# Optimization experiments

Hardware: AMD Instinct MI355X
Metric: run time of the kernel (lower is better)

Reference implementation:

```python
import jax, jax.numpy as jnp
import numpy as np

N_NODES = 50000
N_EDGES = 800000
IN_CH, HID, HEADS, OUT_CH = 16, 64, 4, 8
NEG_SLOPE = 0.2


def _add_self_loops(edge_index, num_nodes):
    loop = jnp.arange(num_nodes, dtype=edge_index.dtype)
    loops = jnp.stack([loop, loop])  # [2, N]
    return jnp.concatenate([edge_index, loops], axis=1)


def _gat_conv(x, src, dst, W, a_src, a_dst, bias, concat):
    """PyG-style GATConv: linear -> per-edge LeakyReLU attention -> segment
    softmax over incoming edges -> scatter-add aggregate."""
    N = x.shape[0]
    H, C = a_src.shape
    h = (x @ W).reshape(N, H, C)                      # [N,H,C]
    alpha_src = (h * a_src).sum(-1)                   # [N,H]
    alpha_dst = (h * a_dst).sum(-1)                   # [N,H]
    e = jax.nn.leaky_relu(alpha_src[src] + alpha_dst[dst], NEG_SLOPE)  # [E,H]
    # numerically stable segment softmax over edges grouped by dst
    e_max = jax.ops.segment_max(e, dst, num_segments=N)
    e_exp = jnp.exp(e - e_max[dst])
    denom = jax.ops.segment_sum(e_exp, dst, num_segments=N)
    alpha = e_exp / denom[dst]                        # [E,H]
    msg = h[src] * alpha[:, :, None]                  # [E,H,C]
    out = jax.ops.segment_sum(msg, dst, num_segments=N)  # [N,H,C]
    if concat:
        return out.reshape(N, H * C) + bias
    return out.mean(axis=1) + bias


def setup_inputs() -> dict:
    key = jax.random.key(0)
    ks = jax.random.split(key, 12)
    s = 0.1
    return {
        "x": jax.random.normal(ks[0], (N_NODES, IN_CH), jnp.float32),
        "edge_index": jax.random.randint(ks[1], (2, N_EDGES), 0, N_NODES, jnp.int64),
        "W1": jax.random.normal(ks[2], (IN_CH, HEADS * HID), jnp.float32) * s,
        "as1": jax.random.normal(ks[3], (HEADS, HID), jnp.float32) * s,
        "ad1": jax.random.normal(ks[4], (HEADS, HID), jnp.float32) * s,
        "b1": jnp.zeros((HEADS * HID,), jnp.float32),
        "W2": jax.random.normal(ks[5], (HEADS * HID, HEADS * HID), jnp.float32) * s,
        "as2": jax.random.normal(ks[6], (HEADS, HID), jnp.float32) * s,
        "ad2": jax.random.normal(ks[7], (HEADS, HID), jnp.float32) * s,
        "b2": jnp.zeros((HID,), jnp.float32),
        "Wc": jax.random.normal(ks[8], (HID, OUT_CH), jnp.float32) * s,
        "bc": jnp.zeros((OUT_CH,), jnp.float32),
    }


def reference(x, edge_index, W1, as1, ad1, b1, W2, as2, ad2, b2, Wc, bc):
    ei = _add_self_loops(edge_index, x.shape[0])
    src, dst = ei[0], ei[1]
    h = _gat_conv(x, src, dst, W1, as1, ad1, b1, concat=True)
    h = jax.nn.elu(h)
    h = _gat_conv(h, src, dst, W2, as2, ad2, b2, concat=False)
    h = jax.nn.elu(h)
    return h @ Wc + bc  # [N, OUT_CH]
```

## Files before the change

kernel.cpp:

```cpp
#include <hip/hip_runtime.h>
#include <math.h>

#define NODES   50000
#define HEADS   4
#define HID     64
#define FDIM    256
#define IN_CH   16
#define NEG_SLOPE 0.2f

typedef unsigned short ushort_t;
typedef unsigned int uint_t;
typedef __attribute__((ext_vector_type(8))) short bf16x8;
typedef __attribute__((ext_vector_type(4))) float f32x4;
typedef __attribute__((ext_vector_type(2))) float f32x2;

__device__ inline ushort_t f2bf(float f) {
    uint_t u = __float_as_uint(f);
    u += 0x7fffu + ((u >> 16) & 1u);
    return (ushort_t)(u >> 16);
}
__device__ inline void unpack2(uint_t u, float& a, float& b) {
    a = __uint_as_float(u << 16);
    b = __uint_as_float(u & 0xffff0000u);
}
__device__ inline uint_t f2h(float f) {
    _Float16 h = (_Float16)f;
    return (uint_t)*(ushort_t*)&h;
}
__device__ inline float h2f(uint_t u) {
    ushort_t us = (ushort_t)u;
    _Float16 h = *(_Float16*)&us;
    return (float)h;
}


__global__ __launch_bounds__(256) void k_prep(const float* __restrict__ x,
                                              const float* __restrict__ W1,
                                              const float* __restrict__ as1,
                                              const float* __restrict__ ad1,
                                              const float* __restrict__ W2,
                                              const int* __restrict__ ei, int E,
                                              ushort_t* __restrict__ h,
                                              float* __restrict__ asrc,
                                              float* __restrict__ adst,
                                              ushort_t* __restrict__ W2T,
                                              int* __restrict__ deg, int Nn) {
    int bid = blockIdx.x, t = threadIdx.x;
    if (bid >= Nn + 256) {
        int e = (bid - Nn - 256) * 256 + t;
        int Etot = E + Nn;
        if (e >= Etot) return;
        int d = (e < E) ? ei[E + e] : (e - E);
        if (d >= 0 && d < Nn) atomicAdd(&deg[d], 1);
        return;
    }
    if (bid >= Nn) {
        int idx = (bid - Nn) * 256 + t;
        int n = idx >> 8, k = idx & 255;
        W2T[idx] = f2bf(W2[k * FDIM + n]);
        return;
    }
    const float4* xp = (const float4*)(x + bid * IN_CH);
    float4 x0 = xp[0], x1 = xp[1], x2 = xp[2], x3 = xp[3];
    float s = x0.x * W1[t]            + x0.y * W1[FDIM + t]
            + x0.z * W1[2 * FDIM + t] + x0.w * W1[3 * FDIM + t]
            + x1.x * W1[4 * FDIM + t] + x1.y * W1[5 * FDIM + t]
            + x1.z * W1[6 * FDIM + t] + x1.w * W1[7 * FDIM + t]
            + x2.x * W1[8 * FDIM + t] + x2.y * W1[9 * FDIM + t]
            + x2.z * W1[10 * FDIM + t]+ x2.w * W1[11 * FDIM + t]
            + x3.x * W1[12 * FDIM + t]+ x3.y * W1[13 * FDIM + t]
            + x3.z * W1[14 * FDIM + t]+ x3.w * W1[15 * FDIM + t];
    h[(long)bid * FDIM + t] = f2bf(s);
    float p1 = s * as1[t];
    float p2 = s * ad1[t];
#pragma unroll
    for (int off = 1; off < 64; off <<= 1) {
        p1 += __shfl_xor(p1, off);
        p2 += __shfl_xor(p2, off);
    }
    if ((t & 63) == 0) {
        int hh = t >> 6;
        asrc[bid * 4 + hh] = p1;
        adst[bid * 4 + hh] = p2;
    }
}


__global__ __launch_bounds__(256) void k_scanA(const int* __restrict__ deg,
                                               int* __restrict__ bsum, int N) {
    __shared__ int sh[256];
    int t = threadIdx.x;
    int i0 = blockIdx.x * 4096 + t * 16;
    int s = 0;
#pragma unroll
    for (int j = 0; j < 16; ++j) s += (i0 + j < N) ? deg[i0 + j] : 0;
    sh[t] = s;
    __syncthreads();
    for (int off = 128; off; off >>= 1) {
        if (t < off) sh[t] += sh[t + off];
        __syncthreads();
    }
    if (t == 0) bsum[blockIdx.x] = sh[0];
}

__global__ void k_scanB(int* __restrict__ bsum, int* __restrict__ rowst, int nb, int N) {
    int t = threadIdx.x;
    int orig = (t < nb) ? bsum[t] : 0;
    int v = orig;
#pragma unroll
    for (int off = 1; off < 64; off <<= 1) {
        int u = __shfl_up(v, off);
        if (t >= off) v += u;
    }
    if (t < nb) bsum[t] = v - orig;
    if (t == 63) rowst[N] = v;
}

__global__ __launch_bounds__(256) void k_scanC(const int* __restrict__ deg,
                                               const int* __restrict__ bsum,
                                               int* __restrict__ rowst,
                                               int* __restrict__ cursor, int N) {
    __shared__ int sh[256];
    int t = threadIdx.x, b = blockIdx.x;
    int i0 = b * 4096 + t * 16;
    int v[16], s = 0;
#pragma unroll
    for (int j = 0; j < 16; ++j) { v[j] = (i0 + j < N) ? deg[i0 + j] : 0; s += v[j]; }
    sh[t] = s;
    __syncthreads();
    for (int off = 1; off < 256; off <<= 1) {
        int u = (t >= off) ? sh[t - off] : 0;
        __syncthreads();
        sh[t] += u;
        __syncthreads();
    }
    int excl = sh[t] - s + bsum[b];
#pragma unroll
    for (int j = 0; j < 16; ++j) {
        if (i0 + j < N) { rowst[i0 + j] = excl; cursor[i0 + j] = excl; }
        excl += v[j];
    }
}

__global__ void k_scatter(const int* __restrict__ ei, int E, int N,
                          int* __restrict__ cursor, int2* __restrict__ csr2) {
    int e = blockIdx.x * blockDim.x + threadIdx.x;
    int Etot = E + N;
    if (e >= Etot) return;
    int s, d;
    if (e < E) { s = ei[e]; d = ei[E + e]; } else { s = d = e - E; }
    if (d < 0 || d >= N) return;
    int pos = atomicAdd(&cursor[d], 1);
    csr2[pos] = make_int2(s, d);
}


__global__ __launch_bounds__(256) void k_gemm2(const ushort_t* __restrict__ A,
                                               const ushort_t* __restrict__ BT,
                                               ushort_t* __restrict__ C, int M) {
    __shared__ short As[64 * 40];
    __shared__ short Bs[64 * 40];
    int tid = threadIdx.x;
    int row0 = blockIdx.y * 64, col0 = blockIdx.x * 64;
    int wid = tid >> 6, lane = tid & 63;
    int wm = wid >> 1, wn = wid & 1;
    int quad = lane >> 4, lm = lane & 15;
    int lr = tid >> 2, lk = (tid & 3) * 8;
    f32x4 acc[2][2] = {};
    for (int k0 = 0; k0 < FDIM; k0 += 32) {
        uint4 av = {0u, 0u, 0u, 0u};
        int ar = row0 + lr;
        if (ar < M) av = *(const uint4*)(A + (long)ar * FDIM + k0 + lk);
        *(uint4*)(&As[lr * 40 + lk]) = av;
        uint4 bv = *(const uint4*)(BT + (long)(col0 + lr) * FDIM + k0 + lk);
        *(uint4*)(&Bs[lr * 40 + lk]) = bv;
        __syncthreads();
        bf16x8 a0 = *(const bf16x8*)(&As[(wm * 32 + lm) * 40 + quad * 8]);
        bf16x8 a1 = *(const bf16x8*)(&As[(wm * 32 + 16 + lm) * 40 + quad * 8]);
        bf16x8 b0 = *(const bf16x8*)(&Bs[(wn * 32 + lm) * 40 + quad * 8]);
        bf16x8 b1 = *(const bf16x8*)(&Bs[(wn * 32 + 16 + lm) * 40 + quad * 8]);
        acc[0][0] = __builtin_amdgcn_mfma_f32_16x16x32_bf16(a0, b0, acc[0][0], 0, 0, 0);
        acc[0][1] = __builtin_amdgcn_mfma_f32_16x16x32_bf16(a0, b1, acc[0][1], 0, 0, 0);
        acc[1][0] = __builtin_amdgcn_mfma_f32_16x16x32_bf16(a1, b0, acc[1][0], 0, 0, 0);
        acc[1][1] = __builtin_amdgcn_mfma_f32_16x16x32_bf16(a1, b1, acc[1][1], 0, 0, 0);
        __syncthreads();
    }
#pragma unroll
    for (int mi = 0; mi < 2; ++mi)
#pragma unroll
        for (int ni = 0; ni < 2; ++ni)
#pragma unroll
            for (int r = 0; r < 4; ++r) {
                int row = row0 + wm * 32 + mi * 16 + quad * 4 + r;
                int col = col0 + wn * 32 + ni * 16 + lm;
                if (row < M) C[(long)row * FDIM + col] = f2bf(acc[mi][ni][r]);
            }
}


__global__ void k_alpha(const ushort_t* __restrict__ h, const float* __restrict__ a_s,
                        const float* __restrict__ a_d, float* __restrict__ asrc,
                        float* __restrict__ adst, int Nn) {
    int idx = blockIdx.x * blockDim.x + threadIdx.x;
    if (idx >= Nn * HEADS) return;
    int n = idx >> 2, hh = idx & 3;
    const uint4* hp = (const uint4*)(h + (long)n * FDIM + hh * HID);
    const float* asp = a_s + hh * HID;
    const float* adp = a_d + hh * HID;
    float s1 = 0.f, s2 = 0.f;
#pragma unroll
    for (int q = 0; q < 8; ++q) {
        uint4 u = hp[q];
        float f[8];
        unpack2(u.x, f[0], f[1]); unpack2(u.y, f[2], f[3]);
        unpack2(u.z, f[4], f[5]); unpack2(u.w, f[6], f[7]);
#pragma unroll
        for (int j = 0; j < 8; ++j) { s1 += f[j] * asp[q * 8 + j]; s2 += f[j] * adp[q * 8 + j]; }
    }
    asrc[idx] = s1;
    adst[idx] = s2;
}


__global__ void k_pw(const int2* __restrict__ csr2, const float* __restrict__ asrc,
                     const float* __restrict__ adst, uint_t* __restrict__ pwb, int Etot) {
    int e = blockIdx.x * blockDim.x + threadIdx.x;
    if (e >= Etot) return;
    int2 sd = csr2[e];
    float4 av = *(const float4*)(asrc + sd.x * 4);
    float4 dv = *(const float4*)(adst + sd.y * 4);
    float t[4] = {av.x + dv.x, av.y + dv.y, av.z + dv.z, av.w + dv.w};
    uint_t sh = (uint_t)sd.x << 16;
#pragma unroll
    for (int h = 0; h < 4; ++h) {
        float tt = (t[h] > 0.f) ? t[h] : NEG_SLOPE * t[h];
        pwb[h * Etot + e] = sh | f2h(__expf(tt));
    }
}


__device__ inline void fma8(f32x2& a0, f32x2& a1, f32x2& a2, f32x2& a3,
                            uint4 hv, float pw) {
    f32x2 p = {pw, pw};
    f32x2 u;
    u.x = __uint_as_float(hv.x << 16); u.y = __uint_as_float(hv.x & 0xffff0000u);
    a0 += p * u;
    u.x = __uint_as_float(hv.y << 16); u.y = __uint_as_float(hv.y & 0xffff0000u);
    a1 += p * u;
    u.x = __uint_as_float(hv.z << 16); u.y = __uint_as_float(hv.z & 0xffff0000u);
    a2 += p * u;
    u.x = __uint_as_float(hv.w << 16); u.y = __uint_as_float(hv.w & 0xffff0000u);
    a3 += p * u;
}

__global__ __launch_bounds__(256) void k_agg(const ushort_t* __restrict__ h,
                                             const uint_t* __restrict__ pwb,
                                             const int* __restrict__ row_start,
                                             const float* __restrict__ b1,
                                             const float* __restrict__ b2,
                                             const float* __restrict__ Wc,
                                             const float* __restrict__ bc,
                                             ushort_t* __restrict__ hout,
                                             float* __restrict__ fout,
                                             int mode, int Etot, int N) {
    __shared__ float zsh[2 * FDIM];
    __shared__ float wsh[584];
    int tid  = threadIdx.x;
    int hh   = tid >> 6;
    int lane = tid & 63;
    int half = lane >> 5;
    int l32  = lane & 31;
    int g    = l32 >> 3;
    int cg   = l32 & 7;
    int d    = blockIdx.x * 2 + half;
    bool valid = d < N;

    if (!mode) {
        for (int i = tid; i < 584; i += 256)
            wsh[i] = (i < 512) ? Wc[i] : ((i < 520) ? bc[i - 512] : b2[i - 520]);
    }

    int s0 = 0, s1 = 0;
    if (valid) { s0 = row_start[d]; s1 = row_start[d + 1]; }
    int cnt  = s1 - s0;
    int maxc = max(cnt, __shfl_xor(cnt, 32));
    const uint_t* pwp = pwb + (long)hh * Etot;
    const char* hbase = (const char*)h + (hh * HID + cg * 8) * 2;

    f32x2 a0 = {0.f, 0.f}, a1 = {0.f, 0.f}, a2 = {0.f, 0.f}, a3 = {0.f, 0.f};
    float den = 0.f;

    for (int off = 0; off < maxc; off += 16) {
        int i0 = s0 + off + g;
        uint_t u0 = (i0      < s1) ? pwp[i0]      : 0u;
        uint_t u1 = (i0 + 4  < s1) ? pwp[i0 + 4]  : 0u;
        uint_t u2 = (i0 + 8  < s1) ? pwp[i0 + 8]  : 0u;
        uint_t u3 = (i0 + 12 < s1) ? pwp[i0 + 12] : 0u;
        uint4 hv0 = *(const uint4*)(hbase + ((size_t)(u0 >> 16) << 9));
        uint4 hv1 = *(const uint4*)(hbase + ((size_t)(u1 >> 16) << 9));
        uint4 hv2 = *(const uint4*)(hbase + ((size_t)(u2 >> 16) << 9));
        uint4 hv3 = *(const uint4*)(hbase + ((size_t)(u3 >> 16) << 9));
        float pw0 = h2f(u0 & 0xffffu), pw1 = h2f(u1 & 0xffffu);
        float pw2 = h2f(u2 & 0xffffu), pw3 = h2f(u3 & 0xffffu);
        den += (pw0 + pw1) + (pw2 + pw3);
        fma8(a0, a1, a2, a3, hv0, pw0);
        fma8(a0, a1, a2, a3, hv1, pw1);
        fma8(a0, a1, a2, a3, hv2, pw2);
        fma8(a0, a1, a2, a3, hv3, pw3);
    }
#pragma unroll
    for (int off = 8; off <= 16; off <<= 1) {
        a0.x += __shfl_xor(a0.x, off); a0.y += __shfl_xor(a0.y, off);
        a1.x += __shfl_xor(a1.x, off); a1.y += __shfl_xor(a1.y, off);
        a2.x += __shfl_xor(a2.x, off); a2.y += __shfl_xor(a2.y, off);
        a3.x += __shfl_xor(a3.x, off); a3.y += __shfl_xor(a3.y, off);
        den  += __shfl_xor(den, off);
    }

    if (mode) {
        if (g == 0 && valid) {
            float inv = 1.f / den;
            float v[8] = {a0.x, a0.y, a1.x, a1.y, a2.x, a2.y, a3.x, a3.y};
            const float* bp = b1 + hh * HID + cg * 8;
#pragma unroll
            for (int j = 0; j < 8; ++j) {
                float t = v[j] * inv + bp[j];
                v[j] = (t > 0.f) ? t : __expf(t) - 1.f;
            }
            uint4 u;
            u.x = (uint_t)f2bf(v[0]) | ((uint_t)f2bf(v[1]) << 16);
            u.y = (uint_t)f2bf(v[2]) | ((uint_t)f2bf(v[3]) << 16);
            u.z = (uint_t)f2bf(v[4]) | ((uint_t)f2bf(v[5]) << 16);
            u.w = (uint_t)f2bf(v[6]) | ((uint_t)f2bf(v[7]) << 16);
            *(uint4*)(hout + (long)d * FDIM + hh * HID + cg * 8) = u;
        }
    } else {
        if (g == 0 && valid) {
            float inv = 1.f / den;
            float v[8] = {a0.x, a0.y, a1.x, a1.y, a2.x, a2.y, a3.x, a3.y};
            int zb = half * FDIM + hh * HID + cg * 8;
#pragma unroll
            for (int j = 0; j < 8; ++j) zsh[zb + j] = v[j] * inv;
        }
        __syncthreads();
        if (tid < 128) {
            int node = tid >> 6, c = tid & 63;
            int dd = blockIdx.x * 2 + node;
            if (dd < N) {
                const float* zp = zsh + node * FDIM;
                float zv = 0.25f * (zp[c] + zp[64 + c] + zp[128 + c] + zp[192 + c])
                         + wsh[520 + c];
                zv = (zv > 0.f) ? zv : __expf(zv) - 1.f;
                zsh[node * FDIM + c] = zv;
            }
        }
        __syncthreads();
        if (tid < 16) {
            int node = tid >> 3, o = tid & 7;
            int dd = blockIdx.x * 2 + node;
            if (dd < N) {
                float acc = wsh[512 + o];
                const float* zp = zsh + node * FDIM;
#pragma unroll 8
                for (int c = 0; c < 64; ++c) acc += zp[c] * wsh[c * 8 + o];
                fout[(long)dd * 8 + o] = acc;
            }
        }
    }
}


extern "C" void kernel_launch(void* const* d_in, const int* in_sizes, int n_in,
                              void* d_out, int out_size, void* d_ws, size_t ws_size,
                              hipStream_t stream) {
    const float* x   = (const float*)d_in[0];
    const int*   ei  = (const int*)d_in[1];
    const float* W1  = (const float*)d_in[2];
    const float* as1 = (const float*)d_in[3];
    const float* ad1 = (const float*)d_in[4];
    const float* b1  = (const float*)d_in[5];
    const float* W2  = (const float*)d_in[6];
    const float* as2 = (const float*)d_in[7];
    const float* ad2 = (const float*)d_in[8];
    const float* b2  = (const float*)d_in[9];
    const float* Wc  = (const float*)d_in[10];
    const float* bc  = (const float*)d_in[11];
    float* out = (float*)d_out;

    const int N = NODES;
    const int E = in_sizes[1] / 2;
    const int Etot = E + N;

    char* ws = (char*)d_ws;
    size_t off = 0;
    auto alloc = [&](size_t bytes) {
        void* p = ws + off;
        off = (off + bytes + 255) & ~(size_t)255;
        return p;
    };
    ushort_t* hbf    = (ushort_t*)alloc((size_t)N * FDIM * 2);
    ushort_t* hact   = (ushort_t*)alloc((size_t)N * FDIM * 2);
    float*    asrc   = (float*)alloc((size_t)N * HEADS * 4);
    float*    adst   = (float*)alloc((size_t)N * HEADS * 4);
    ushort_t* W2T    = (ushort_t*)alloc((size_t)FDIM * FDIM * 2);
    int*      deg    = (int*)alloc((size_t)N * 4);
    int*      rowst  = (int*)alloc((size_t)(N + 1) * 4);
    int*      cursor = (int*)alloc((size_t)N * 4);
    int*      bsum   = (int*)alloc(64 * 4);
    int2*     csr2   = (int2*)alloc((size_t)Etot * 8);
    uint_t*   pwb    = (uint_t*)alloc((size_t)Etot * HEADS * 4);

    const int tpb = 256;
    int egrid = (Etot + tpb - 1) / tpb;
    int nb = (N + 4095) / 4096;

    hipMemsetAsync(deg, 0, (size_t)N * 4, stream);

    k_prep<<<N + 256 + egrid, tpb, 0, stream>>>(x, W1, as1, ad1, W2, ei, E,
                                                hbf, asrc, adst, W2T, deg, N);
    k_scanA<<<nb, 256, 0, stream>>>(deg, bsum, N);
    k_scanB<<<1, 64, 0, stream>>>(bsum, rowst, nb, N);
    k_scanC<<<nb, 256, 0, stream>>>(deg, bsum, rowst, cursor, N);
    k_scatter<<<egrid, tpb, 0, stream>>>(ei, E, N, cursor, csr2);

    k_pw<<<egrid, tpb, 0, stream>>>(csr2, asrc, adst, pwb, Etot);
    k_agg<<<(N + 1) / 2, 256, 0, stream>>>(hbf, pwb, rowst, b1, nullptr, nullptr, nullptr,
                                           hact, nullptr, 1, Etot, N);

    dim3 g2(FDIM / 64, (N + 63) / 64);
    k_gemm2<<<g2, 256, 0, stream>>>(hact, W2T, hbf, N);
    k_alpha<<<(N * HEADS + tpb - 1) / tpb, tpb, 0, stream>>>(hbf, as2, ad2, asrc, adst, N);
    k_pw<<<egrid, tpb, 0, stream>>>(csr2, asrc, adst, pwb, Etot);
    k_agg<<<(N + 1) / 2, 256, 0, stream>>>(hbf, pwb, rowst, nullptr, b2, Wc, bc,
                                           nullptr, out, 0, Etot, N);
}
```

Before: 400.6 us.

## Fuse layer-2 attention logits into GEMM epilogue and batch nodes in prep

The layer-2 attention dot products (asrc/adst) are now computed in the bf16 MFMA GEMM epilogue from fp32 accumulators, using shuffle reductions and a small shared buffer, so the separate k_alpha kernel and its re-read of h are gone. Each GEMM column block is exactly one head, so it writes one head's logits directly. Separately, k_prep now handles 8 nodes per block with W1 columns held in registers, and writes bf16 pairs as 32-bit stores. The epilogue adds a sync and shuffles, and the logits now come from unrounded fp32 accumulators rather than bf16 values, which changes numerics slightly.

```diff
diff --git a/kernel.cpp b/kernel.cpp
--- a/kernel.cpp
+++ b/kernel.cpp
@@ -18,10 +18,6 @@
     uint_t u = __float_as_uint(f);
     u += 0x7fffu + ((u >> 16) & 1u);
     return (ushort_t)(u >> 16);
-}
-__device__ inline void unpack2(uint_t u, float& a, float& b) {
-    a = __uint_as_float(u << 16);
-    b = __uint_as_float(u & 0xffff0000u);
 }
 __device__ inline uint_t f2h(float f) {
     _Float16 h = (_Float16)f;
@@ -44,44 +40,50 @@
                                               float* __restrict__ asrc,
                                               float* __restrict__ adst,
                                               ushort_t* __restrict__ W2T,
-                                              int* __restrict__ deg, int Nn) {
+                                              int* __restrict__ deg, int Nn, int NB) {
     int bid = blockIdx.x, t = threadIdx.x;
-    if (bid >= Nn + 256) {
-        int e = (bid - Nn - 256) * 256 + t;
+    if (bid >= NB + 256) {
+        int e = (bid - NB - 256) * 256 + t;
         int Etot = E + Nn;
         if (e >= Etot) return;
         int d = (e < E) ? ei[E + e] : (e - E);
         if (d >= 0 && d < Nn) atomicAdd(&deg[d], 1);
         return;
     }
-    if (bid >= Nn) {
-        int idx = (bid - Nn) * 256 + t;
+    if (bid >= NB) {
+        int idx = (bid - NB) * 256 + t;
         int n = idx >> 8, k = idx & 255;
         W2T[idx] = f2bf(W2[k * FDIM + n]);
         return;
     }
-    const float4* xp = (const float4*)(x + bid * IN_CH);
-    float4 x0 = xp[0], x1 = xp[1], x2 = xp[2], x3 = xp[3];
-    float s = x0.x * W1[t]            + x0.y * W1[FDIM + t]
-            + x0.z * W1[2 * FDIM + t] + x0.w * W1[3 * FDIM + t]
-            + x1.x * W1[4 * FDIM + t] + x1.y * W1[5 * FDIM + t]
-            + x1.z * W1[6 * FDIM + t] + x1.w * W1[7 * FDIM + t]
-            + x2.x * W1[8 * FDIM + t] + x2.y * W1[9 * FDIM + t]
-            + x2.z * W1[10 * FDIM + t]+ x2.w * W1[11 * FDIM + t]
-            + x3.x * W1[12 * FDIM + t]+ x3.y * W1[13 * FDIM + t]
-            + x3.z * W1[14 * FDIM + t]+ x3.w * W1[15 * FDIM + t];
-    h[(long)bid * FDIM + t] = f2bf(s);
-    float p1 = s * as1[t];
-    float p2 = s * ad1[t];
-#pragma unroll
-    for (int off = 1; off < 64; off <<= 1) {
-        p1 += __shfl_xor(p1, off);
-        p2 += __shfl_xor(p2, off);
-    }
-    if ((t & 63) == 0) {
-        int hh = t >> 6;
-        asrc[bid * 4 + hh] = p1;
-        adst[bid * 4 + hh] = p2;
+    float w1c[16];
+#pragma unroll
+    for (int k = 0; k < 16; ++k) w1c[k] = W1[k * FDIM + t];
+    float av = as1[t], dv = ad1[t];
+    int hh = t >> 6;
+#pragma unroll
+    for (int j = 0; j < 8; ++j) {
+        int n = bid * 8 + j;
+        if (n >= Nn) break;
+        const float4* xp = (const float4*)(x + n * IN_CH);
+        float4 x0 = xp[0], x1 = xp[1], x2 = xp[2], x3 = xp[3];
+        float s = x0.x * w1c[0]  + x0.y * w1c[1]  + x0.z * w1c[2]  + x0.w * w1c[3]
+                + x1.x * w1c[4]  + x1.y * w1c[5]  + x1.z * w1c[6]  + x1.w * w1c[7]
+                + x2.x * w1c[8]  + x2.y * w1c[9]  + x2.z * w1c[10] + x2.w * w1c[11]
+                + x3.x * w1c[12] + x3.y * w1c[13] + x3.z * w1c[14] + x3.w * w1c[15];
+        uint_t pv = (uint_t)f2bf(s);
+        uint_t ov = __shfl_down(pv, 1);
+        if (!(t & 1)) *(uint_t*)(h + (long)n * FDIM + t) = pv | (ov << 16);
+        float p1 = s * av, p2 = s * dv;
+#pragma unroll
+        for (int off = 1; off < 64; off <<= 1) {
+            p1 += __shfl_xor(p1, off);
+            p2 += __shfl_xor(p2, off);
+        }
+        if ((t & 63) == 0) {
+            asrc[n * 4 + hh] = p1;
+            adst[n * 4 + hh] = p2;
+        }
     }
 }
 
@@ -157,9 +159,14 @@
 
 __global__ __launch_bounds__(256) void k_gemm2(const ushort_t* __restrict__ A,
                                                const ushort_t* __restrict__ BT,
-                                               ushort_t* __restrict__ C, int M) {
+                                               const float* __restrict__ as2,
+                                               const float* __restrict__ ad2,
+                                               ushort_t* __restrict__ C,
+                                               float* __restrict__ asrc,
+                                               float* __restrict__ adst, int M) {
     __shared__ short As[64 * 40];
     __shared__ short Bs[64 * 40];
+    __shared__ float2 red[64][2];
     int tid = threadIdx.x;
     int row0 = blockIdx.y * 64, col0 = blockIdx.x * 64;
     int wid = tid >> 6, lane = tid & 63;
@@ -195,30 +202,30 @@
                 int col = col0 + wn * 32 + ni * 16 + lm;
                 if (row < M) C[(long)row * FDIM + col] = f2bf(acc[mi][ni][r]);
             }
-}
-
-
-__global__ void k_alpha(const ushort_t* __restrict__ h, const float* __restrict__ a_s,
-                        const float* __restrict__ a_d, float* __restrict__ asrc,
-                        float* __restrict__ adst, int Nn) {
-    int idx = blockIdx.x * blockDim.x + threadIdx.x;
-    if (idx >= Nn * HEADS) return;
-    int n = idx >> 2, hh = idx & 3;
-    const uint4* hp = (const uint4*)(h + (long)n * FDIM + hh * HID);
-    const float* asp = a_s + hh * HID;
-    const float* adp = a_d + hh * HID;
-    float s1 = 0.f, s2 = 0.f;
-#pragma unroll
-    for (int q = 0; q < 8; ++q) {
-        uint4 u = hp[q];
-        float f[8];
-        unpack2(u.x, f[0], f[1]); unpack2(u.y, f[2], f[3]);
-        unpack2(u.z, f[4], f[5]); unpack2(u.w, f[6], f[7]);
-#pragma unroll
-        for (int j = 0; j < 8; ++j) { s1 += f[j] * asp[q * 8 + j]; s2 += f[j] * adp[q * 8 + j]; }
-    }
-    asrc[idx] = s1;
-    adst[idx] = s2;
+    float asv0 = as2[col0 + wn * 32 + lm], asv1 = as2[col0 + wn * 32 + 16 + lm];
+    float adv0 = ad2[col0 + wn * 32 + lm], adv1 = ad2[col0 + wn * 32 + 16 + lm];
+#pragma unroll
+    for (int mi = 0; mi < 2; ++mi)
+#pragma unroll
+        for (int r = 0; r < 4; ++r) {
+            float ps = acc[mi][0][r] * asv0 + acc[mi][1][r] * asv1;
+            float pd = acc[mi][0][r] * adv0 + acc[mi][1][r] * adv1;
+#pragma unroll
+            for (int off = 1; off < 16; off <<= 1) {
+                ps += __shfl_xor(ps, off);
+                pd += __shfl_xor(pd, off);
+            }
+            if (lm == 0) red[wm * 32 + mi * 16 + quad * 4 + r][wn] = make_float2(ps, pd);
+        }
+    __syncthreads();
+    if (tid < 64) {
+        int row = row0 + tid;
+        if (row < M) {
+            float2 e0 = red[tid][0], e1 = red[tid][1];
+            asrc[row * 4 + blockIdx.x] = e0.x + e1.x;
+            adst[row * 4 + blockIdx.x] = e0.y + e1.y;
+        }
+    }
 }
 
 
@@ -413,11 +420,12 @@
     const int tpb = 256;
     int egrid = (Etot + tpb - 1) / tpb;
     int nb = (N + 4095) / 4096;
+    int NB = (N + 7) / 8;
 
     hipMemsetAsync(deg, 0, (size_t)N * 4, stream);
 
-    k_prep<<<N + 256 + egrid, tpb, 0, stream>>>(x, W1, as1, ad1, W2, ei, E,
-                                                hbf, asrc, adst, W2T, deg, N);
+    k_prep<<<NB + 256 + egrid, tpb, 0, stream>>>(x, W1, as1, ad1, W2, ei, E,
+                                                 hbf, asrc, adst, W2T, deg, N, NB);
     k_scanA<<<nb, 256, 0, stream>>>(deg, bsum, N);
     k_scanB<<<1, 64, 0, stream>>>(bsum, rowst, nb, N);
     k_scanC<<<nb, 256, 0, stream>>>(deg, bsum, rowst, cursor, N);
@@ -428,8 +436,7 @@
                                            hact, nullptr, 1, Etot, N);
 
     dim3 g2(FDIM / 64, (N + 63) / 64);
-    k_gemm2<<<g2, 256, 0, stream>>>(hact, W2T, hbf, N);
-    k_alpha<<<(N * HEADS + tpb - 1) / tpb, tpb, 0, stream>>>(hbf, as2, ad2, asrc, adst, N);
+    k_gemm2<<<g2, 256, 0, stream>>>(hact, W2T, as2, ad2, hbf, asrc, adst, N);
     k_pw<<<egrid, tpb, 0, stream>>>(csr2, asrc, adst, pwb, Etot);
     k_agg<<<(N + 1) / 2, 256, 0, stream>>>(hbf, pwb, rowst, nullptr, b2, Wc, bc,
                                            nullptr, out, 0, Etot, N);
```

Measured after the change: 380.1 us. 1.05x faster.
